# Kernel optimization log

Hardware: AMD Instinct MI355X
Metric: run time of the kernel (lower is better)

The kernel has to match this reference:

```python
import jax, jax.numpy as jnp
import numpy as np

N = 16000
E = 128000
IN_DIM = 512
H1 = 4096
H2 = 1024
OUT_DIM = 64


def setup_inputs() -> dict:
    key = jax.random.key(0)
    ks = jax.random.split(key, 8)
    x = jax.random.normal(ks[0], (N, IN_DIM), dtype=jnp.float32)
    edge_index = jax.random.randint(ks[1], (2, E), 0, N, dtype=jnp.int64)

    def glorot(k, fan_in, fan_out):
        lim = float(np.sqrt(6.0 / (fan_in + fan_out)))
        return jax.random.uniform(k, (fan_in, fan_out), jnp.float32, -lim, lim)

    # PyG SAGEConv: out = lin_l(mean_j x_j) + lin_r(x); lin_l has bias, lin_r does not.
    params = {
        'W1l': glorot(ks[2], IN_DIM, H1), 'b1': jnp.zeros((H1,), jnp.float32),
        'W1r': glorot(ks[3], IN_DIM, H1),
        'W2l': glorot(ks[4], H1, H2), 'b2': jnp.zeros((H2,), jnp.float32),
        'W2r': glorot(ks[5], H1, H2),
        'W3l': glorot(ks[6], H2, OUT_DIM), 'b3': jnp.zeros((OUT_DIM,), jnp.float32),
        'W3r': glorot(ks[7], H2, OUT_DIM),
    }
    return {'x': x, 'edge_index': edge_index, **params}


def _sage_conv(x, src, dst, Wl, b, Wr):
    # mean-aggregate neighbor features at dst, then linear; plus root transform
    agg = jax.ops.segment_sum(x[src], dst, num_segments=N)          # [N, F_in]
    cnt = jax.ops.segment_sum(jnp.ones((src.shape[0],), x.dtype), dst, num_segments=N)
    mean = agg / jnp.maximum(cnt, 1.0)[:, None]
    return mean @ Wl + b + x @ Wr


def reference(x, edge_index, W1l, b1, W1r, W2l, b2, W2r, W3l, b3, W3r):
    src, dst = edge_index[0], edge_index[1]
    h = jax.nn.relu(_sage_conv(x, src, dst, W1l, b1, W1r))   # dropout is identity in eval
    h = jax.nn.relu(_sage_conv(h, src, dst, W2l, b2, W2r))
    h = _sage_conv(h, src, dst, W3l, b3, W3r)
    return jax.nn.log_softmax(h, axis=1)
```

## Files before the change

### kernel.cpp

```cpp
#include <hip/hip_runtime.h>
#include <stdint.h>

typedef __bf16 bf16x8 __attribute__((ext_vector_type(8)));
typedef float  f32x4  __attribute__((ext_vector_type(4)));
typedef unsigned short u16x8 __attribute__((ext_vector_type(8)));
typedef const void __attribute__((address_space(1))) gv_t;
typedef void __attribute__((address_space(3))) sv_t;

static __device__ __forceinline__ unsigned short f2bf(float f) {
  unsigned u = __float_as_uint(f);
  u += 0x7fffu + ((u >> 16) & 1u);
  return (unsigned short)(u >> 16);
}
static __device__ __forceinline__ float bf2f(unsigned short h) {
  return __uint_as_float(((unsigned)h) << 16);
}
static __device__ __forceinline__ void gload16(const void* g, void* l) {
  __builtin_amdgcn_global_load_lds((gv_t*)g, (sv_t*)l, 16, 0, 0);
}

__global__ void k_sentinel(float* out, int n, float val) {
  int t = blockIdx.x * 256 + threadIdx.x;
  if (t < n) out[t] = val;
}

static __device__ __forceinline__ void transW_tile(const float* W, unsigned short* Wt,
                                                   int K, int N, int ld, int kofs,
                                                   int n0, int k0, float (*tile)[33]) {
  int tx = threadIdx.x & 31, ty = threadIdx.x >> 5;
#pragma unroll
  for (int r = 0; r < 4; ++r)
    tile[ty + r * 8][tx] = W[(size_t)(k0 + ty + r * 8) * N + n0 + tx];
  __syncthreads();
#pragma unroll
  for (int r = 0; r < 4; ++r)
    Wt[(size_t)(n0 + ty + r * 8) * ld + kofs + k0 + tx] = f2bf(tile[tx][ty + r * 8]);
}

__global__ void k_prep(const float4* __restrict__ x, ushort4* __restrict__ xm,
                       const float* W1l, const float* W1r, const float* W2l,
                       const float* W2r, const float* W3l, const float* W3r,
                       unsigned short* W1t, unsigned short* W2t, unsigned short* W3t,
                       int* deg, int Nn) {
  __shared__ float tile[32][33];
  int bid = blockIdx.x;
  if (bid < 8000) {
    int t = bid * 256 + threadIdx.x;
    int row = t >> 7, c = t & 127;
    float4 v = x[t];
    xm[(size_t)row * 256 + c] = make_ushort4(f2bf(v.x), f2bf(v.y), f2bf(v.z), f2bf(v.w));
    return;
  }
  bid -= 8000;
  if (bid < 2048) {
    transW_tile(W1r, W1t, 512, 4096, 1024, 0, (bid & 127) * 32, (bid >> 7) * 32, tile);
    return;
  }
  bid -= 2048;
  if (bid < 2048) {
    transW_tile(W1l, W1t, 512, 4096, 1024, 512, (bid & 127) * 32, (bid >> 7) * 32, tile);
    return;
  }
  bid -= 2048;
  if (bid < 4096) {
    transW_tile(W2l, W2t, 4096, 1024, 4096, 0, (bid & 31) * 32, (bid >> 5) * 32, tile);
    return;
  }
  bid -= 4096;
  if (bid < 4096) {
    transW_tile(W2r, W2t + (size_t)1024 * 4096, 4096, 1024, 4096, 0, (bid & 31) * 32,
                (bid >> 5) * 32, tile);
    return;
  }
  bid -= 4096;
  if (bid < 64) {
    transW_tile(W3l, W3t, 1024, 64, 1024, 0, (bid & 1) * 32, (bid >> 1) * 32, tile);
    return;
  }
  bid -= 64;
  if (bid < 64) {
    transW_tile(W3r, W3t + (size_t)64 * 1024, 1024, 64, 1024, 0, (bid & 1) * 32,
                (bid >> 1) * 32, tile);
    return;
  }
  bid -= 64;
  {
    int t = bid * 256 + threadIdx.x;
    if (t < Nn) deg[t] = 0;
  }
}

static __device__ __forceinline__ int detect_i64(const int* ei) {
  __shared__ int sflag;
  if (threadIdx.x < 64) {
    int bad = 0;
#pragma unroll
    for (int j = 0; j < 4; ++j) bad |= ei[2 * (threadIdx.x * 4 + j) + 1];
    unsigned long long m = __ballot(bad != 0);
    if (threadIdx.x == 0) sflag = (m == 0ull) ? 1 : 0;
  }
  __syncthreads();
  return sflag;
}

__global__ void k_degree(const int* ei, int E, int* deg) {
  int f = detect_i64(ei);
  int t = blockIdx.x * 256 + threadIdx.x;
  if (t < E) {
    int d = f ? ei[2 * (E + t)] : ei[E + t];
    atomicAdd(&deg[d], 1);
  }
}
__global__ void k_scan(const int* deg, int* rp, int* cur, int n) {
  __shared__ int ssum[256];
  int t = threadIdx.x;
  int chunk = (n + 255) >> 8;
  int lo = t * chunk, hi = min(lo + chunk, n);
  int s = 0;
  for (int i = lo; i < hi; ++i) s += deg[i];
  ssum[t] = s;
  __syncthreads();
  if (t == 0) {
    int run = 0;
    for (int i = 0; i < 256; ++i) { int v = ssum[i]; ssum[i] = run; run += v; }
  }
  __syncthreads();
  int run = ssum[t];
  for (int i = lo; i < hi; ++i) { rp[i] = run; cur[i] = run; run += deg[i]; }
  if (t == 255) rp[n] = run;
}
__global__ void k_fill(const int* ei, int E, int* cur, int* col) {
  int f = detect_i64(ei);
  int t = blockIdx.x * 256 + threadIdx.x;
  if (t < E) {
    int s = f ? ei[2 * t] : ei[t];
    int d = f ? ei[2 * (E + t)] : ei[E + t];
    int p = atomicAdd(&cur[d], 1);
    col[p] = s;
  }
}

__global__ void k_agg(unsigned short* __restrict__ xm, const int* __restrict__ rp,
                      const int* __restrict__ col) {
  int i = blockIdx.x;
  int s = rp[i], e = rp[i + 1];
  float inv = 1.0f / (float)max(e - s, 1);
  int f8 = threadIdx.x & 63;
  int p = threadIdx.x >> 6;
  const u16x8* xm8 = (const u16x8*)xm;
  float acc[8] = {0.f, 0.f, 0.f, 0.f, 0.f, 0.f, 0.f, 0.f};
  for (int n = s + p; n < e; n += 4) {
    u16x8 v = xm8[(size_t)col[n] * 128 + f8];
#pragma unroll
    for (int j = 0; j < 8; ++j) acc[j] += bf2f(v[j]);
  }
  __shared__ float red[3][64][8];
  if (p > 0) {
#pragma unroll
    for (int j = 0; j < 8; ++j) red[p - 1][f8][j] = acc[j];
  }
  __syncthreads();
  if (p == 0) {
    u16x8 o;
#pragma unroll
    for (int j = 0; j < 8; ++j) {
      float v = (acc[j] + red[0][f8][j] + red[1][f8][j] + red[2][f8][j]) * inv;
      o[j] = f2bf(v);
    }
    ((u16x8*)xm)[(size_t)i * 128 + 64 + f8] = o;
  }
}

#define XCD_SWZ(bnShift_)                                                             \
  const int nwg = gridDim.x;                                                          \
  const int q8 = nwg >> 3, r8 = nwg & 7;                                              \
  const int xcd = blockIdx.x & 7, idx = blockIdx.x >> 3;                              \
  const int wg = (xcd < r8 ? xcd * (q8 + 1) : r8 * (q8 + 1) + (xcd - r8) * q8) + idx; \
  const int bn = wg & ((1 << (bnShift_)) - 1);                                        \
  const int bm = wg >> (bnShift_);

#define VMCNT(NUM) asm volatile("s_waitcnt vmcnt(" #NUM ")" ::: "memory")

#define STAGE_A(BUF, I, K0)                                            \
  gload16(Ap + (size_t)((I) * 64 + rsub) * K + (K0) + sl8,             \
          (char*)&lds[BUF][0][0] + ((I) * 64 + wq * 8) * 128)
#define STAGE_B(BUF, I, K0)                                            \
  gload16(Bp + (size_t)((I) * 64 + rsub) * K + (K0) + sl8,             \
          (char*)&lds[BUF][1][0] + ((I) * 64 + wq * 8) * 128)
#define LOAD_AFR(DST, CUR, QA)                                                          \
  do {                                                                                  \
    const char* baseA = (const char*)&lds[CUR][0][0];                                   \
    _Pragma("unroll") for (int mm = 0; mm < 4; ++mm) {                                  \
      const int rr = ((QA) * 4 + mm) * 32 + wr * 16 + (lane & 15);                      \
      _Pragma("unroll") for (int kk = 0; kk < 2; ++kk)                                  \
          DST[mm][kk] = *(const bf16x8*)(baseA + rr * 128 +                             \
                                         (((kk * 4 + (lane >> 4)) ^ (lane & 7)) << 4)); \
    }                                                                                   \
  } while (0)
#define LOAD_BFR(DST, CUR, QB)                                                          \
  do {                                                                                  \
    const char* baseB = (const char*)&lds[CUR][1][0];                                   \
    _Pragma("unroll") for (int nn = 0; nn < 2; ++nn) {                                  \
      const int cc = ((QB) * 2 + nn) * 64 + wc * 16 + (lane & 15);                      \
      _Pragma("unroll") for (int kk = 0; kk < 2; ++kk)                                  \
          DST[nn][kk] = *(const bf16x8*)(baseB + cc * 128 +                             \
                                         (((kk * 4 + (lane >> 4)) ^ (lane & 7)) << 4)); \
    }                                                                                   \
  } while (0)
#define MFMA_Q(QA, QB, AFR, BFR)                                                        \
  do {                                                                                  \
    _Pragma("unroll") for (int mm = 0; mm < 4; ++mm)                                    \
        _Pragma("unroll") for (int nn = 0; nn < 2; ++nn)                                \
            _Pragma("unroll") for (int kk = 0; kk < 2; ++kk)                            \
                acc[(QA) * 4 + mm][(QB) * 2 + nn] =                                     \
                    __builtin_amdgcn_mfma_f32_16x16x32_bf16(                            \
                        AFR[mm][kk], BFR[nn][kk], acc[(QA) * 4 + mm][(QB) * 2 + nn],    \
                        0, 0, 0);                                                       \
  } while (0)

template <bool RELU, bool BIAS>
__global__ __launch_bounds__(512, 1) void k_gemm256(
    const unsigned short* __restrict__ A, const unsigned short* __restrict__ B,
    const float* __restrict__ bias, unsigned short* __restrict__ outp,
    int Mreal, int N, int K, int bnShift) {
  __shared__ __align__(16) unsigned short lds[2][2][256 * 64];
  const int tid = threadIdx.x;
  const int lane = tid & 63;
  const int wq = tid >> 6;
  const int wr = wq >> 2;
  const int wc = wq & 3;
  XCD_SWZ(bnShift)
  const unsigned short* Ap = A + (size_t)bm * 256 * K;
  const unsigned short* Bp = B + (size_t)bn * 256 * K;
  const int sl8 = ((lane & 7) ^ (lane >> 3)) * 8;
  const int rsub = wq * 8 + (lane >> 3);

  f32x4 acc[8][4];
#pragma unroll
  for (int m = 0; m < 8; ++m)
#pragma unroll
    for (int n = 0; n < 4; ++n) acc[m][n] = (f32x4){0.f, 0.f, 0.f, 0.f};

  STAGE_A(0, 0, 0); STAGE_A(0, 1, 0);
  STAGE_B(0, 0, 0); STAGE_B(0, 1, 0);
  STAGE_B(0, 2, 0); STAGE_B(0, 3, 0);
  STAGE_A(0, 2, 0); STAGE_A(0, 3, 0);
  STAGE_A(1, 0, 64); STAGE_A(1, 1, 64);
  STAGE_B(1, 0, 64); STAGE_B(1, 1, 64);
  STAGE_B(1, 2, 64); STAGE_B(1, 3, 64);
  STAGE_A(1, 2, 64); STAGE_A(1, 3, 64);
  VMCNT(8);
  __builtin_amdgcn_s_barrier();

  bf16x8 a0[4][2], b0[2][2], a1[4][2], b1[2][2];
  LOAD_AFR(a0, 0, 0);
  LOAD_BFR(b0, 0, 0);

  const int nt = K >> 6;
#pragma unroll 1
  for (int t = 0; t < nt; ++t) {
    const int cur = t & 1, nxt = cur ^ 1;
    const int k2 = (t + 2) << 6;
    LOAD_AFR(a1, cur, 1);
    LOAD_BFR(b1, cur, 1);
    __builtin_amdgcn_s_setprio(1);
    MFMA_Q(0, 0, a0, b0);
    MFMA_Q(0, 1, a0, b1);
    __builtin_amdgcn_s_setprio(0);
    asm volatile("s_waitcnt vmcnt(0) lgkmcnt(0)" ::: "memory");
    __builtin_amdgcn_s_barrier();
    if (t + 2 < nt) {
      STAGE_A(cur, 0, k2); STAGE_A(cur, 1, k2);
      STAGE_B(cur, 0, k2); STAGE_B(cur, 1, k2);
      STAGE_B(cur, 2, k2); STAGE_B(cur, 3, k2);
      STAGE_A(cur, 2, k2); STAGE_A(cur, 3, k2);
    }
    __builtin_amdgcn_s_setprio(1);
    MFMA_Q(1, 0, a1, b0);
    MFMA_Q(1, 1, a1, b1);
    __builtin_amdgcn_s_setprio(0);
    if (t + 1 < nt) {
      LOAD_AFR(a0, nxt, 0);
      LOAD_BFR(b0, nxt, 0);
    }
  }

  const int row0 = bm * 256 + wr * 16 + ((lane >> 4) << 2);
  const int col0 = bn * 256 + wc * 16 + (lane & 15);
  const bool full = (bm + 1) * 256 <= Mreal;
#pragma unroll
  for (int m = 0; m < 8; ++m) {
#pragma unroll
    for (int n = 0; n < 4; ++n) {
      const int col = col0 + n * 64;
      float bb = BIAS ? bias[col] : 0.f;
      if (full) {
#pragma unroll
        for (int r = 0; r < 4; ++r) {
          int row = row0 + m * 32 + r;
          float v = acc[m][n][r] + bb;
          if (RELU) v = fmaxf(v, 0.f);
          outp[(size_t)row * N + col] = f2bf(v);
        }
      } else {
#pragma unroll
        for (int r = 0; r < 4; ++r) {
          int row = row0 + m * 32 + r;
          if (row < Mreal) {
            float v = acc[m][n][r] + bb;
            if (RELU) v = fmaxf(v, 0.f);
            outp[(size_t)row * N + col] = f2bf(v);
          }
        }
      }
    }
  }
}

#define STAGE1_A(BUF, I, K0)                                           \
  gload16(Ap + (size_t)((I) * 32 + rsub) * K + (K0) + sl8,             \
          (char*)&lds[BUF][0][0] + ((I) * 32 + wq * 8) * 128)
#define STAGE1_B(BUF, I, K0)                                           \
  gload16(Bp + (size_t)((I) * 32 + rsub) * K + (K0) + sl8,             \
          (char*)&lds[BUF][1][0] + ((I) * 32 + wq * 8) * 128)
#define LOAD1_AFR(DST, CUR, QA)                                                         \
  do {                                                                                  \
    const char* baseA = (const char*)&lds[CUR][0][0];                                   \
    _Pragma("unroll") for (int mm = 0; mm < 2; ++mm) {                                  \
      const int rr = wr * 64 + ((QA) * 2 + mm) * 16 + (lane & 15);                      \
      _Pragma("unroll") for (int kk = 0; kk < 2; ++kk)                                  \
          DST[mm][kk] = *(const bf16x8*)(baseA + rr * 128 +                             \
                                         (((kk * 4 + (lane >> 4)) ^ (lane & 7)) << 4)); \
    }                                                                                   \
  } while (0)
#define LOAD1_BFR(DST, CUR, QB)                                                         \
  do {                                                                                  \
    const char* baseB = (const char*)&lds[CUR][1][0];                                   \
    _Pragma("unroll") for (int nn = 0; nn < 2; ++nn) {                                  \
      const int cc = wc * 64 + ((QB) * 2 + nn) * 16 + (lane & 15);                      \
      _Pragma("unroll") for (int kk = 0; kk < 2; ++kk)                                  \
          DST[nn][kk] = *(const bf16x8*)(baseB + cc * 128 +                             \
                                         (((kk * 4 + (lane >> 4)) ^ (lane & 7)) << 4)); \
    }                                                                                   \
  } while (0)
#define MFMA1_Q(QA, QB, AFR, BFR)                                                       \
  do {                                                                                  \
    _Pragma("unroll") for (int mm = 0; mm < 2; ++mm)                                    \
        _Pragma("unroll") for (int nn = 0; nn < 2; ++nn)                                \
            _Pragma("unroll") for (int kk = 0; kk < 2; ++kk)                            \
                acc[(QA) * 2 + mm][(QB) * 2 + nn] =                                     \
                    __builtin_amdgcn_mfma_f32_16x16x32_bf16(                            \
                        AFR[mm][kk], BFR[nn][kk], acc[(QA) * 2 + mm][(QB) * 2 + nn],    \
                        0, 0, 0);                                                       \
  } while (0)

template <bool RELU, bool BIAS>
__global__ __launch_bounds__(256, 1) void k_gemm128(
    const unsigned short* __restrict__ A, const unsigned short* __restrict__ B,
    const float* __restrict__ bias, unsigned short* __restrict__ outp,
    int Mreal, int N, int K, int bnShift) {
  __shared__ __align__(16) unsigned short lds[2][2][128 * 64];
  const int tid = threadIdx.x;
  const int lane = tid & 63;
  const int wq = tid >> 6;
  const int wr = wq >> 1;
  const int wc = wq & 1;
  XCD_SWZ(bnShift)
  const unsigned short* Ap = A + (size_t)bm * 128 * K;
  const unsigned short* Bp = B + (size_t)bn * 128 * K;
  const int sl8 = ((lane & 7) ^ (lane >> 3)) * 8;
  const int rsub = wq * 8 + (lane >> 3);

  f32x4 acc[4][4];
#pragma unroll
  for (int m = 0; m < 4; ++m)
#pragma unroll
    for (int n = 0; n < 4; ++n) acc[m][n] = (f32x4){0.f, 0.f, 0.f, 0.f};

  STAGE1_A(0, 0, 0); STAGE1_A(0, 1, 0);
  STAGE1_B(0, 0, 0); STAGE1_B(0, 1, 0);
  STAGE1_B(0, 2, 0); STAGE1_B(0, 3, 0);
  STAGE1_A(0, 2, 0); STAGE1_A(0, 3, 0);
  STAGE1_A(1, 0, 64); STAGE1_A(1, 1, 64);
  STAGE1_B(1, 0, 64); STAGE1_B(1, 1, 64);
  STAGE1_B(1, 2, 64); STAGE1_B(1, 3, 64);
  STAGE1_A(1, 2, 64); STAGE1_A(1, 3, 64);
  VMCNT(8);
  __builtin_amdgcn_s_barrier();

  bf16x8 a0[2][2], b0[2][2], a1[2][2], b1[2][2];
  LOAD1_AFR(a0, 0, 0);
  LOAD1_BFR(b0, 0, 0);

  const int nt = K >> 6;
#pragma unroll 1
  for (int t = 0; t < nt; ++t) {
    const int cur = t & 1, nxt = cur ^ 1;
    const int k2 = (t + 2) << 6;
    LOAD1_AFR(a1, cur, 1);
    LOAD1_BFR(b1, cur, 1);
    __builtin_amdgcn_s_setprio(1);
    MFMA1_Q(0, 0, a0, b0);
    MFMA1_Q(0, 1, a0, b1);
    __builtin_amdgcn_s_setprio(0);
    asm volatile("s_waitcnt vmcnt(0) lgkmcnt(0)" ::: "memory");
    __builtin_amdgcn_s_barrier();
    if (t + 2 < nt) {
      STAGE1_A(cur, 0, k2); STAGE1_A(cur, 1, k2);
      STAGE1_B(cur, 0, k2); STAGE1_B(cur, 1, k2);
      STAGE1_B(cur, 2, k2); STAGE1_B(cur, 3, k2);
      STAGE1_A(cur, 2, k2); STAGE1_A(cur, 3, k2);
    }
    __builtin_amdgcn_s_setprio(1);
    MFMA1_Q(1, 0, a1, b0);
    MFMA1_Q(1, 1, a1, b1);
    __builtin_amdgcn_s_setprio(0);
    if (t + 1 < nt) {
      LOAD1_AFR(a0, nxt, 0);
      LOAD1_BFR(b0, nxt, 0);
    }
  }

  const int row0 = bm * 128 + wr * 64 + ((lane >> 4) << 2);
  const int col0 = bn * 128 + wc * 64 + (lane & 15);
  const bool full = (bm + 1) * 128 <= Mreal;
#pragma unroll
  for (int m = 0; m < 4; ++m) {
#pragma unroll
    for (int n = 0; n < 4; ++n) {
      const int col = col0 + n * 16;
      float bb = BIAS ? bias[col] : 0.f;
      if (full) {
#pragma unroll
        for (int r = 0; r < 4; ++r) {
          int row = row0 + m * 16 + r;
          float v = acc[m][n][r] + bb;
          if (RELU) v = fmaxf(v, 0.f);
          outp[(size_t)row * N + col] = f2bf(v);
        }
      } else {
#pragma unroll
        for (int r = 0; r < 4; ++r) {
          int row = row0 + m * 16 + r;
          if (row < Mreal) {
            float v = acc[m][n][r] + bb;
            if (RELU) v = fmaxf(v, 0.f);
            outp[(size_t)row * N + col] = f2bf(v);
          }
        }
      }
    }
  }
}

template <int NF, bool TWO, bool RELU, bool BIAS>
__global__ __launch_bounds__(256) void k_gemm(
    const unsigned short* __restrict__ Am, const unsigned short* __restrict__ Ar,
    const unsigned short* __restrict__ Bl, const unsigned short* __restrict__ Br,
    const float* __restrict__ bias, unsigned short* __restrict__ outp, int N, int K) {
  constexpr int BN = NF * 32;
  __shared__ __align__(16) unsigned short lds[(128 + BN) * 64];
  unsigned short* ldsA = lds;
  unsigned short* ldsB = lds + 128 * 64;

  const int tid = threadIdx.x;
  const int lane = tid & 63;
  const int w = tid >> 6;
  const int wr = w >> 1, wc = w & 1;

  f32x4 zero = {0.f, 0.f, 0.f, 0.f};
  f32x4 acc[4][NF];
#pragma unroll
  for (int m = 0; m < 4; ++m)
#pragma unroll
    for (int n = 0; n < NF; ++n) acc[m][n] = zero;

  const int bm = blockIdx.x, bn = blockIdx.y;
  const int sl_st = (lane & 7) ^ (lane >> 3);

#pragma unroll 1
  for (int pass = 0; pass < (TWO ? 2 : 1); ++pass) {
    const unsigned short* A = (TWO && pass) ? Ar : Am;
    const unsigned short* B = (TWO && pass) ? Br : Bl;
    A += (size_t)bm * 128 * K;
    B += (size_t)bn * BN * K;
#pragma unroll 1
    for (int k0 = 0; k0 < K; k0 += 64) {
      __syncthreads();
#pragma unroll
      for (int q = 0; q < 4; ++q) {
        int rowi = (w * 4 + q) * 8 + (lane >> 3);
        gload16(A + (size_t)rowi * K + k0 + sl_st * 8, (char*)ldsA + (w * 4 + q) * 1024);
      }
#pragma unroll
      for (int q = 0; q < NF; ++q) {
        int rowi = (w * NF + q) * 8 + (lane >> 3);
        gload16(B + (size_t)rowi * K + k0 + sl_st * 8, (char*)ldsB + (w * NF + q) * 1024);
      }
      __syncthreads();
#pragma unroll
      for (int kk = 0; kk < 2; ++kk) {
        int sw = (((kk * 4 + (lane >> 4)) ^ (lane & 7)) << 4);
        bf16x8 af[4], bfr[NF];
#pragma unroll
        for (int m = 0; m < 4; ++m) {
          int r = wr * 64 + m * 16 + (lane & 15);
          af[m] = *(const bf16x8*)((const char*)ldsA + r * 128 + sw);
        }
#pragma unroll
        for (int n = 0; n < NF; ++n) {
          int c = wc * (BN / 2) + n * 16 + (lane & 15);
          bfr[n] = *(const bf16x8*)((const char*)ldsB + c * 128 + sw);
        }
#pragma unroll
        for (int m = 0; m < 4; ++m)
#pragma unroll
          for (int n = 0; n < NF; ++n)
            acc[m][n] = __builtin_amdgcn_mfma_f32_16x16x32_bf16(af[m], bfr[n], acc[m][n], 0, 0, 0);
      }
    }
  }

  const int row0 = bm * 128 + wr * 64;
  const int col0 = bn * BN + wc * (BN / 2);
#pragma unroll
  for (int m = 0; m < 4; ++m) {
#pragma unroll
    for (int n = 0; n < NF; ++n) {
      int col = col0 + n * 16 + (lane & 15);
      float bb = BIAS ? bias[col] : 0.f;
#pragma unroll
      for (int r = 0; r < 4; ++r) {
        int row = row0 + m * 16 + ((lane >> 4) << 2) + r;
        float v = acc[m][n][r] + bb;
        if (RELU) v = fmaxf(v, 0.f);
        outp[(size_t)row * N + col] = f2bf(v);
      }
    }
  }
}

__global__ void k_combine2(const unsigned short* __restrict__ Z2, const int* __restrict__ rp,
                           const int* __restrict__ col, const float* __restrict__ bias,
                           unsigned short* __restrict__ h2) {
  int i = blockIdx.x;
  int s = rp[i], e = rp[i + 1];
  float inv = 1.0f / (float)max(e - s, 1);
  int f8 = threadIdx.x & 127;
  int p = threadIdx.x >> 7;
  const u16x8* Z28 = (const u16x8*)Z2;
  float acc[8] = {0.f, 0.f, 0.f, 0.f, 0.f, 0.f, 0.f, 0.f};
  for (int n = s + p; n < e; n += 2) {
    u16x8 v = Z28[(size_t)col[n] * 256 + f8];
#pragma unroll
    for (int j = 0; j < 8; ++j) acc[j] += bf2f(v[j]);
  }
  __shared__ float red[128][8];
  if (p == 1) {
#pragma unroll
    for (int j = 0; j < 8; ++j) red[f8][j] = acc[j];
  }
  __syncthreads();
  if (p == 0) {
    u16x8 r = Z28[(size_t)i * 256 + 128 + f8];
    float4 b4a = ((const float4*)bias)[f8 * 2];
    float4 b4b = ((const float4*)bias)[f8 * 2 + 1];
    float bb[8] = {b4a.x, b4a.y, b4a.z, b4a.w, b4b.x, b4b.y, b4b.z, b4b.w};
    u16x8 o;
#pragma unroll
    for (int j = 0; j < 8; ++j) {
      float v = (acc[j] + red[f8][j]) * inv + bf2f(r[j]) + bb[j];
      o[j] = f2bf(fmaxf(v, 0.f));
    }
    ((u16x8*)h2)[(size_t)i * 128 + f8] = o;
  }
}

__global__ void k_combine3(const unsigned short* __restrict__ Z3, const int* __restrict__ rp,
                           const int* __restrict__ col, const float* __restrict__ bias,
                           float* __restrict__ out) {
  int i = blockIdx.x * 4 + (threadIdx.x >> 6);
  int c = threadIdx.x & 63;
  int s = rp[i], e = rp[i + 1];
  float inv = 1.0f / (float)max(e - s, 1);
  float a = 0.f;
  for (int n = s; n < e; ++n) a += bf2f(Z3[(size_t)col[n] * 128 + c]);
  float v = a * inv + bf2f(Z3[(size_t)i * 128 + 64 + c]) + bias[c];
  float m = v;
#pragma unroll
  for (int o = 1; o < 64; o <<= 1) m = fmaxf(m, __shfl_xor(m, o, 64));
  float t = expf(v - m);
  float sum = t;
#pragma unroll
  for (int o = 1; o < 64; o <<= 1) sum += __shfl_xor(sum, o, 64);
  out[(size_t)i * 64 + c] = (v - m) - logf(sum);
}

extern "C" void kernel_launch(void* const* d_in, const int* in_sizes, int n_in,
                              void* d_out, int out_size, void* d_ws, size_t ws_size,
                              hipStream_t stream) {
  const float* x   = (const float*)d_in[0];
  const int*   ei  = (const int*)d_in[1];
  const float* W1l = (const float*)d_in[2];
  const float* b1  = (const float*)d_in[3];
  const float* W1r = (const float*)d_in[4];
  const float* W2l = (const float*)d_in[5];
  const float* b2  = (const float*)d_in[6];
  const float* W2r = (const float*)d_in[7];
  const float* W3l = (const float*)d_in[8];
  const float* b3  = (const float*)d_in[9];
  const float* W3r = (const float*)d_in[10];

  const int Nn = 16000;
  const int E = in_sizes[1] / 2;

  char* p = (char*)d_ws;
  auto carve = [&](size_t bytes) {
    char* r = p;
    p += (bytes + 255) & ~(size_t)255;
    return r;
  };
  int* deg    = (int*)carve((size_t)Nn * 4);
  int* rp     = (int*)carve((size_t)(Nn + 1) * 4);
  int* cur    = (int*)carve((size_t)Nn * 4);
  int* colidx = (int*)carve((size_t)E * 4);
  unsigned short* W2t = (unsigned short*)carve((size_t)2048 * 4096 * 2);
  unsigned short* W3t = (unsigned short*)carve((size_t)128 * 1024 * 2);
  unsigned short* xm  = (unsigned short*)carve((size_t)Nn * 1024 * 2);
  unsigned short* h1  = (unsigned short*)carve((size_t)Nn * 4096 * 2);
  unsigned short* Z2  = (unsigned short*)carve((size_t)Nn * 2048 * 2);
  unsigned short* Z3  = (unsigned short*)carve((size_t)Nn * 128 * 2);
  unsigned short* h2  = xm;
  unsigned short* W1t = Z2;

  size_t need = (size_t)(p - (char*)d_ws);
  if (ws_size < need) {
    k_sentinel<<<(out_size + 255) / 256, 256, 0, stream>>>((float*)d_out, out_size,
                                                           (float)(ws_size >> 20));
    return;
  }

  k_prep<<<8000 + 2048 + 2048 + 4096 + 4096 + 64 + 64 + 63, 256, 0, stream>>>(
      (const float4*)x, (ushort4*)xm, W1l, W1r, W2l, W2r, W3l, W3r, W1t, W2t, W3t, deg, Nn);
  k_degree<<<(E + 255) / 256, 256, 0, stream>>>(ei, E, deg);
  k_scan<<<1, 256, 0, stream>>>(deg, rp, cur, Nn);
  k_fill<<<(E + 255) / 256, 256, 0, stream>>>(ei, E, cur, colidx);
  k_agg<<<Nn, 256, 0, stream>>>(xm, rp, colidx);
  k_gemm128<true, true><<<125 * 32, 256, 0, stream>>>(xm, W1t, b1, h1, Nn, 4096, 1024, 5);
  k_gemm256<false, false><<<63 * 8, 512, 0, stream>>>(h1, W2t, nullptr, Z2, Nn, 2048, 4096, 3);
  k_combine2<<<Nn, 256, 0, stream>>>(Z2, rp, colidx, b2, h2);
  k_gemm<2, false, false, false><<<dim3(125, 2), 256, 0, stream>>>(h2, nullptr, W3t, nullptr,
                                                                   nullptr, Z3, 128, 1024);
  k_combine3<<<Nn / 4, 256, 0, stream>>>(Z3, rp, colidx, b3, (float*)d_out);

  (void)n_in; (void)out_size;
}
```

Baseline: 575.7 us.

## Replace layer-1 128x128 GEMM with 256x256-tile kernel using 32x32x16 MFMA

The first-layer GEMM (N=16000, K=1024, 4096 outputs) moves from a 128x128-tile, 4-wave kernel with 16x16x32 MFMAs to a 256x256-tile, 8-wave kernel using 32x32x16 bf16 MFMAs with 16-wide accumulators. Larger tiles halve global/LDS traffic per FLOP and the bigger MFMA shape cuts LDS fragment reads per MFMA. The cost is fewer workgroups (1008 vs 4000), which can hurt tail balance given 16000 rows pad to 63 tiles, plus more register pressure and a different LDS read swizzle. Shared staging code is factored into macros.

```diff
diff --git a/kernel.cpp b/kernel.cpp
--- a/kernel.cpp
+++ b/kernel.cpp
@@ -3,6 +3,7 @@
 
 typedef __bf16 bf16x8 __attribute__((ext_vector_type(8)));
 typedef float  f32x4  __attribute__((ext_vector_type(4)));
+typedef float  f32x16 __attribute__((ext_vector_type(16)));
 typedef unsigned short u16x8 __attribute__((ext_vector_type(8)));
 typedef const void __attribute__((address_space(1))) gv_t;
 typedef void __attribute__((address_space(3))) sv_t;
@@ -187,6 +188,27 @@
 #define STAGE_B(BUF, I, K0)                                            \
   gload16(Bp + (size_t)((I) * 64 + rsub) * K + (K0) + sl8,             \
           (char*)&lds[BUF][1][0] + ((I) * 64 + wq * 8) * 128)
+
+#define GEMM256_PRO                                                     \
+  STAGE_A(0, 0, 0); STAGE_A(0, 1, 0);                                   \
+  STAGE_B(0, 0, 0); STAGE_B(0, 1, 0);                                   \
+  STAGE_B(0, 2, 0); STAGE_B(0, 3, 0);                                   \
+  STAGE_A(0, 2, 0); STAGE_A(0, 3, 0);                                   \
+  STAGE_A(1, 0, 64); STAGE_A(1, 1, 64);                                 \
+  STAGE_B(1, 0, 64); STAGE_B(1, 1, 64);                                 \
+  STAGE_B(1, 2, 64); STAGE_B(1, 3, 64);                                 \
+  STAGE_A(1, 2, 64); STAGE_A(1, 3, 64);                                 \
+  VMCNT(8);                                                             \
+  __builtin_amdgcn_s_barrier();
+
+#define GEMM256_STAGE_NEXT                                              \
+  if (t + 2 < nt) {                                                     \
+    STAGE_A(cur, 0, k2); STAGE_A(cur, 1, k2);                           \
+    STAGE_B(cur, 0, k2); STAGE_B(cur, 1, k2);                           \
+    STAGE_B(cur, 2, k2); STAGE_B(cur, 3, k2);                           \
+    STAGE_A(cur, 2, k2); STAGE_A(cur, 3, k2);                           \
+  }
+
 #define LOAD_AFR(DST, CUR, QA)                                                          \
   do {                                                                                  \
     const char* baseA = (const char*)&lds[CUR][0][0];                                   \
@@ -241,16 +263,7 @@
 #pragma unroll
     for (int n = 0; n < 4; ++n) acc[m][n] = (f32x4){0.f, 0.f, 0.f, 0.f};
 
-  STAGE_A(0, 0, 0); STAGE_A(0, 1, 0);
-  STAGE_B(0, 0, 0); STAGE_B(0, 1, 0);
-  STAGE_B(0, 2, 0); STAGE_B(0, 3, 0);
-  STAGE_A(0, 2, 0); STAGE_A(0, 3, 0);
-  STAGE_A(1, 0, 64); STAGE_A(1, 1, 64);
-  STAGE_B(1, 0, 64); STAGE_B(1, 1, 64);
-  STAGE_B(1, 2, 64); STAGE_B(1, 3, 64);
-  STAGE_A(1, 2, 64); STAGE_A(1, 3, 64);
-  VMCNT(8);
-  __builtin_amdgcn_s_barrier();
+  GEMM256_PRO
 
   bf16x8 a0[4][2], b0[2][2], a1[4][2], b1[2][2];
   LOAD_AFR(a0, 0, 0);
@@ -269,12 +282,7 @@
     __builtin_amdgcn_s_setprio(0);
     asm volatile("s_waitcnt vmcnt(0) lgkmcnt(0)" ::: "memory");
     __builtin_amdgcn_s_barrier();
-    if (t + 2 < nt) {
-      STAGE_A(cur, 0, k2); STAGE_A(cur, 1, k2);
-      STAGE_B(cur, 0, k2); STAGE_B(cur, 1, k2);
-      STAGE_B(cur, 2, k2); STAGE_B(cur, 3, k2);
-      STAGE_A(cur, 2, k2); STAGE_A(cur, 3, k2);
-    }
+    GEMM256_STAGE_NEXT
     __builtin_amdgcn_s_setprio(1);
     MFMA_Q(1, 0, a1, b0);
     MFMA_Q(1, 1, a1, b1);
@@ -317,131 +325,108 @@
   }
 }
 
-#define STAGE1_A(BUF, I, K0)                                           \
-  gload16(Ap + (size_t)((I) * 32 + rsub) * K + (K0) + sl8,             \
-          (char*)&lds[BUF][0][0] + ((I) * 32 + wq * 8) * 128)
-#define STAGE1_B(BUF, I, K0)                                           \
-  gload16(Bp + (size_t)((I) * 32 + rsub) * K + (K0) + sl8,             \
-          (char*)&lds[BUF][1][0] + ((I) * 32 + wq * 8) * 128)
-#define LOAD1_AFR(DST, CUR, QA)                                                         \
+#define LOADW_AFR(DST, CUR, QA)                                                         \
   do {                                                                                  \
     const char* baseA = (const char*)&lds[CUR][0][0];                                   \
     _Pragma("unroll") for (int mm = 0; mm < 2; ++mm) {                                  \
-      const int rr = wr * 64 + ((QA) * 2 + mm) * 16 + (lane & 15);                      \
-      _Pragma("unroll") for (int kk = 0; kk < 2; ++kk)                                  \
-          DST[mm][kk] = *(const bf16x8*)(baseA + rr * 128 +                             \
-                                         (((kk * 4 + (lane >> 4)) ^ (lane & 7)) << 4)); \
+      const int rr = wr * 128 + ((QA) * 2 + mm) * 32 + (lane & 31);                     \
+      _Pragma("unroll") for (int ks = 0; ks < 4; ++ks)                                  \
+          DST[mm][ks] = *(const bf16x8*)(baseA + rr * 128 +                             \
+                                         (((ks * 2 + (lane >> 5)) ^ (lane & 7)) << 4)); \
     }                                                                                   \
   } while (0)
-#define LOAD1_BFR(DST, CUR, QB)                                                         \
+#define LOADW_BFR(DST, CUR, QB)                                                         \
   do {                                                                                  \
     const char* baseB = (const char*)&lds[CUR][1][0];                                   \
-    _Pragma("unroll") for (int nn = 0; nn < 2; ++nn) {                                  \
-      const int cc = wc * 64 + ((QB) * 2 + nn) * 16 + (lane & 15);                      \
-      _Pragma("unroll") for (int kk = 0; kk < 2; ++kk)                                  \
-          DST[nn][kk] = *(const bf16x8*)(baseB + cc * 128 +                             \
-                                         (((kk * 4 + (lane >> 4)) ^ (lane & 7)) << 4)); \
-    }                                                                                   \
+    const int cc = wc * 64 + (QB) * 32 + (lane & 31);                                   \
+    _Pragma("unroll") for (int ks = 0; ks < 4; ++ks)                                    \
+        DST[ks] = *(const bf16x8*)(baseB + cc * 128 +                                   \
+                                   (((ks * 2 + (lane >> 5)) ^ (lane & 7)) << 4));       \
   } while (0)
-#define MFMA1_Q(QA, QB, AFR, BFR)                                                       \
+#define MFMAW_Q(QA, QB, AFR, BFR)                                                       \
   do {                                                                                  \
     _Pragma("unroll") for (int mm = 0; mm < 2; ++mm)                                    \
-        _Pragma("unroll") for (int nn = 0; nn < 2; ++nn)                                \
-            _Pragma("unroll") for (int kk = 0; kk < 2; ++kk)                            \
-                acc[(QA) * 2 + mm][(QB) * 2 + nn] =                                     \
-                    __builtin_amdgcn_mfma_f32_16x16x32_bf16(                            \
-                        AFR[mm][kk], BFR[nn][kk], acc[(QA) * 2 + mm][(QB) * 2 + nn],    \
-                        0, 0, 0);                                                       \
+        _Pragma("unroll") for (int ks = 0; ks < 4; ++ks)                                \
+            acc[(QA) * 2 + mm][QB] = __builtin_amdgcn_mfma_f32_32x32x16_bf16(           \
+                AFR[mm][ks], BFR[ks], acc[(QA) * 2 + mm][QB], 0, 0, 0);                 \
   } while (0)
 
 template <bool RELU, bool BIAS>
-__global__ __launch_bounds__(256, 1) void k_gemm128(
+__global__ __launch_bounds__(512, 1) void k_gemm256w(
     const unsigned short* __restrict__ A, const unsigned short* __restrict__ B,
     const float* __restrict__ bias, unsigned short* __restrict__ outp,
     int Mreal, int N, int K, int bnShift) {
-  __shared__ __align__(16) unsigned short lds[2][2][128 * 64];
+  __shared__ __align__(16) unsigned short lds[2][2][256 * 64];
   const int tid = threadIdx.x;
   const int lane = tid & 63;
   const int wq = tid >> 6;
-  const int wr = wq >> 1;
-  const int wc = wq & 1;
+  const int wr = wq >> 2;
+  const int wc = wq & 3;
   XCD_SWZ(bnShift)
-  const unsigned short* Ap = A + (size_t)bm * 128 * K;
-  const unsigned short* Bp = B + (size_t)bn * 128 * K;
+  const unsigned short* Ap = A + (size_t)bm * 256 * K;
+  const unsigned short* Bp = B + (size_t)bn * 256 * K;
   const int sl8 = ((lane & 7) ^ (lane >> 3)) * 8;
   const int rsub = wq * 8 + (lane >> 3);
 
-  f32x4 acc[4][4];
+  f32x16 acc[4][2];
 #pragma unroll
   for (int m = 0; m < 4; ++m)
 #pragma unroll
-    for (int n = 0; n < 4; ++n) acc[m][n] = (f32x4){0.f, 0.f, 0.f, 0.f};
-
-  STAGE1_A(0, 0, 0); STAGE1_A(0, 1, 0);
-  STAGE1_B(0, 0, 0); STAGE1_B(0, 1, 0);
-  STAGE1_B(0, 2, 0); STAGE1_B(0, 3, 0);
-  STAGE1_A(0, 2, 0); STAGE1_A(0, 3, 0);
-  STAGE1_A(1, 0, 64); STAGE1_A(1, 1, 64);
-  STAGE1_B(1, 0, 64); STAGE1_B(1, 1, 64);
-  STAGE1_B(1, 2, 64); STAGE1_B(1, 3, 64);
-  STAGE1_A(1, 2, 64); STAGE1_A(1, 3, 64);
-  VMCNT(8);
-  __builtin_amdgcn_s_barrier();
-
-  bf16x8 a0[2][2], b0[2][2], a1[2][2], b1[2][2];
-  LOAD1_AFR(a0, 0, 0);
-  LOAD1_BFR(b0, 0, 0);
+    for (int n = 0; n < 2; ++n)
+#pragma unroll
+      for (int r = 0; r < 16; ++r) acc[m][n][r] = 0.f;
+
+  GEMM256_PRO
+
+  bf16x8 a0[2][4], b0[4], a1[2][4], b1[4];
+  LOADW_AFR(a0, 0, 0);
+  LOADW_BFR(b0, 0, 0);
 
   const int nt = K >> 6;
 #pragma unroll 1
   for (int t = 0; t < nt; ++t) {
     const int cur = t & 1, nxt = cur ^ 1;
     const int k2 = (t + 2) << 6;
-    LOAD1_AFR(a1, cur, 1);
-    LOAD1_BFR(b1, cur, 1);
+    LOADW_AFR(a1, cur, 1);
+    LOADW_BFR(b1, cur, 1);
     __builtin_amdgcn_s_setprio(1);
-    MFMA1_Q(0, 0, a0, b0);
-    MFMA1_Q(0, 1, a0, b1);
+    MFMAW_Q(0, 0, a0, b0);
+    MFMAW_Q(0, 1, a0, b1);
     __builtin_amdgcn_s_setprio(0);
     asm volatile("s_waitcnt vmcnt(0) lgkmcnt(0)" ::: "memory");
     __builtin_amdgcn_s_barrier();
-    if (t + 2 < nt) {
-      STAGE1_A(cur, 0, k2); STAGE1_A(cur, 1, k2);
-      STAGE1_B(cur, 0, k2); STAGE1_B(cur, 1, k2);
-      STAGE1_B(cur, 2, k2); STAGE1_B(cur, 3, k2);
-      STAGE1_A(cur, 2, k2); STAGE1_A(cur, 3, k2);
-    }
+    GEMM256_STAGE_NEXT
     __builtin_amdgcn_s_setprio(1);
-    MFMA1_Q(1, 0, a1, b0);
-    MFMA1_Q(1, 1, a1, b1);
+    MFMAW_Q(1, 0, a1, b0);
+    MFMAW_Q(1, 1, a1, b1);
     __builtin_amdgcn_s_setprio(0);
     if (t + 1 < nt) {
-      LOAD1_AFR(a0, nxt, 0);
-      LOAD1_BFR(b0, nxt, 0);
-    }
-  }
-
-  const int row0 = bm * 128 + wr * 64 + ((lane >> 4) << 2);
-  const int col0 = bn * 128 + wc * 64 + (lane & 15);
-  const bool full = (bm + 1) * 128 <= Mreal;
+      LOADW_AFR(a0, nxt, 0);
+      LOADW_BFR(b0, nxt, 0);
+    }
+  }
+
+  const int rbase = bm * 256 + wr * 128 + ((lane >> 5) << 2);
+  const int col0 = bn * 256 + wc * 64 + (lane & 31);
+  const bool full = (bm + 1) * 256 <= Mreal;
 #pragma unroll
   for (int m = 0; m < 4; ++m) {
 #pragma unroll
-    for (int n = 0; n < 4; ++n) {
-      const int col = col0 + n * 16;
+    for (int n = 0; n < 2; ++n) {
+      const int col = col0 + n * 32;
       float bb = BIAS ? bias[col] : 0.f;
       if (full) {
 #pragma unroll
-        for (int r = 0; r < 4; ++r) {
-          int row = row0 + m * 16 + r;
+        for (int r = 0; r < 16; ++r) {
+          int row = rbase + m * 32 + (r & 3) + 8 * (r >> 2);
           float v = acc[m][n][r] + bb;
           if (RELU) v = fmaxf(v, 0.f);
           outp[(size_t)row * N + col] = f2bf(v);
         }
       } else {
 #pragma unroll
-        for (int r = 0; r < 4; ++r) {
-          int row = row0 + m * 16 + r;
+        for (int r = 0; r < 16; ++r) {
+          int row = rbase + m * 32 + (r & 3) + 8 * (r >> 2);
           if (row < Mreal) {
             float v = acc[m][n][r] + bb;
             if (RELU) v = fmaxf(v, 0.f);
@@ -646,7 +631,7 @@
   k_scan<<<1, 256, 0, stream>>>(deg, rp, cur, Nn);
   k_fill<<<(E + 255) / 256, 256, 0, stream>>>(ei, E, cur, colidx);
   k_agg<<<Nn, 256, 0, stream>>>(xm, rp, colidx);
-  k_gemm128<true, true><<<125 * 32, 256, 0, stream>>>(xm, W1t, b1, h1, Nn, 4096, 1024, 5);
+  k_gemm256w<true, true><<<63 * 16, 512, 0, stream>>>(xm, W1t, b1, h1, Nn, 4096, 1024, 4);
   k_gemm256<false, false><<<63 * 8, 512, 0, stream>>>(h1, W2t, nullptr, Z2, Nn, 2048, 4096, 3);
   k_combine2<<<Nn, 256, 0, stream>>>(Z2, rp, colidx, b2, h2);
   k_gemm<2, false, false, false><<<dim3(125, 2), 256, 0, stream>>>(h2, nullptr, W3t, nullptr,
```

Result: faster. 548.6 us (-4.7%).
